# Performance work log

Hardware: AMD Instinct MI355X
Metric: run time of the kernel (lower is better)

Reference implementation:

```python
import jax, jax.numpy as jnp
import numpy as np

B, N, D, R = 4, 50000, 64, 500
E_PER = 62500
E = B * E_PER


def _build_edges():
    rng = np.random.default_rng(0)
    idx = np.repeat(np.arange(B), E_PER)
    vi = rng.integers(0, N, E)
    vj = rng.integers(0, N, E)
    order = np.lexsort((vj, vi, idx))
    idx, vi, vj = idx[order], vi[order], vj[order]
    rel = rng.integers(0, R, E)
    key_vi = idx.astype(np.int64) * N + vi
    _, idx_vi = np.unique(key_vi, return_inverse=True)  # sorted -> nondecreasing segment ids
    key_vj = idx.astype(np.int64) * N + vj
    _, idx_vj = np.unique(key_vj, return_inverse=True)
    all_keys = np.concatenate([key_vi, key_vj])
    uniq_all, inv = np.unique(all_keys, return_inverse=True)
    e2vi, e2vj = inv[:E], inv[E:]
    sel = np.stack([idx, vi, vj, rel, idx_vi, idx_vj, e2vi, e2vj], axis=1).astype(np.int32)
    return sel, int(idx_vi.max() + 1), int(idx_vj.max() + 1), int(len(uniq_all))


def setup_inputs() -> dict:
    sel, n_vi_seg, n_vj_seg, n_visited = _build_edges()
    key = jax.random.key(0)
    ks = jax.random.split(key, 9)
    na = jax.random.uniform(ks[0], (B, N), jnp.float32) + 1e-6
    na = na / jnp.sum(na, axis=1, keepdims=True)
    return {
        'node_attention': na,
        'selected_edges': jnp.asarray(sel),
        'edges_y': jax.random.uniform(ks[1], (E,), jnp.float32, 0.1, 1.0),
        'hidden_con': jax.random.normal(ks[2], (n_visited, D), jnp.float32) * 0.1,
        'hidden_uncon': jax.random.normal(ks[3], (1, N, D), jnp.float32) * 0.1,
        'rel_emb': jax.random.normal(ks[4], (R, D), jnp.float32) * 0.1,
        'ws': jax.random.normal(ks[5], (8, D), jnp.float32) * (1.0 / np.sqrt(8.0)),
        'b': jax.random.normal(ks[6], (D,), jnp.float32) * 0.01,
        'out_w': jax.random.normal(ks[7], (D,), jnp.float32) * 0.3,
        'out_b': jax.random.normal(ks[8], (D,), jnp.float32) * 0.01,
        'n_vi_seg': n_vi_seg,
        'n_vj_seg': n_vj_seg,
    }


def reference(node_attention, selected_edges, edges_y, hidden_con, hidden_uncon,
              rel_emb, ws, b, out_w, out_b, n_vi_seg, n_vj_seg):
    idx, vi, vj = selected_edges[:, 0], selected_edges[:, 1], selected_edges[:, 2]
    rel, idx_vi, idx_vj = selected_edges[:, 3], selected_edges[:, 4], selected_edges[:, 5]
    e2vi, e2vj = selected_edges[:, 6], selected_edges[:, 7]

    # Node2Edge gathers
    hc_vi, hc_vj = hidden_con[e2vi], hidden_con[e2vj]        # [E, D]
    hu = hidden_uncon[0]                                     # hidden_uncon has batch 1
    hu_vi, hu_vj = hu[vi], hu[vj]                            # [E, D]
    re = rel_emb[rel]                                        # [E, D]

    # F layer: interact = [[0,3],[0,2,3],[0,4],[0,2,4],[1,3],[1,2,3],[1,4],[1,2,4]]
    terms = (hc_vi * hc_vj, hc_vi * re * hc_vj, hc_vi * hu_vj, hc_vi * re * hu_vj,
             hu_vi * hc_vj, hu_vi * re * hc_vj, hu_vi * hu_vj, hu_vi * re * hu_vj)
    f = b
    for k in range(8):
        f = f + ws[k] * terms[k]
    f = jax.nn.relu(f) * out_w + out_b                       # [E, D]
    logits = jnp.sum(f, axis=1)                              # [E]

    # NeighborSoftmax at='vi' (segment softmax)
    seg_max = jax.ops.segment_max(logits, idx_vi, num_segments=n_vi_seg)
    e = jnp.exp(logits - seg_max[idx_vi])
    es = jax.ops.segment_sum(e, idx_vi, num_segments=n_vi_seg)
    transition = e / es[idx_vi]

    # attention flow
    na_e = node_attention[idx, vi]
    ta = na_e * transition * edges_y

    # Aggregate at='vj', sum, then scatter into (B, n_nodes)
    aggr = jax.ops.segment_sum(ta, idx_vj, num_segments=n_vj_seg)
    seg_idx = jax.ops.segment_max(idx, idx_vj, num_segments=n_vj_seg)
    seg_vj = jax.ops.segment_max(vj, idx_vj, num_segments=n_vj_seg)
    Bn, Nn = node_attention.shape
    new_att = jnp.zeros((Bn, Nn), node_attention.dtype).at[seg_idx, seg_vj].add(aggr)
    return new_att / jnp.sum(new_att, axis=1, keepdims=True)
```

## Files before the change

kernel.cpp:

```cpp
#include <hip/hip_runtime.h>
#include <math.h>

#define D 64

__global__ __launch_bounds__(256) void k_logits(
    const int* __restrict__ sel, const float* __restrict__ hc,
    const float* __restrict__ hu, const float* __restrict__ re,
    const float* __restrict__ wsm, const float* __restrict__ bias,
    const float* __restrict__ out_w, const float* __restrict__ out_b,
    float* __restrict__ logits, int* __restrict__ seg_start,
    float* __restrict__ out, float* __restrict__ row_sum,
    int E, int BN, int Bn)
{
    const int tid = blockIdx.x * 256 + threadIdx.x;
    const int nthreads = gridDim.x * 256;

    for (int i = tid; i < BN; i += nthreads) out[i] = 0.f;
    if (tid < Bn) row_sum[tid] = 0.f;

    const int lane = threadIdx.x & 63;
    const int g    = lane >> 4;
    const int d16  = lane & 15;

    const float4* wsm4 = (const float4*)wsm;
    float4 W[8];
    #pragma unroll
    for (int k = 0; k < 8; ++k) W[k] = wsm4[k * 16 + d16];
    const float4 Bv = ((const float4*)bias)[d16];
    const float4 Ow = ((const float4*)out_w)[d16];
    const float4 Ob = ((const float4*)out_b)[d16];
    const float* Wf  = (const float*)W;
    const float* Bvf = (const float*)&Bv;
    const float* Owf = (const float*)&Ow;
    const float* Obf = (const float*)&Ob;

    const float4* hc4 = (const float4*)hc;
    const float4* hu4 = (const float4*)hu;
    const float4* re4 = (const float4*)re;

    const int wave   = tid >> 6;
    const int nwaves = nthreads >> 6;
    const int octs   = (E + 7) >> 3;

    for (int q = wave; q < octs; q += nwaves) {
        const int e0 = q * 8 + g;
        const int e1 = q * 8 + 4 + g;
        const bool v0 = (e0 < E);
        const bool v1 = (e1 < E);
        const int ec0 = v0 ? e0 : (E - 1);
        const int ec1 = v1 ? e1 : (E - 1);

        const int4 sA0 = *(const int4*)(sel + (size_t)ec0 * 8);
        const int4 sB0 = *(const int4*)(sel + (size_t)ec0 * 8 + 4);
        const int4 sA1 = *(const int4*)(sel + (size_t)ec1 * 8);
        const int4 sB1 = *(const int4*)(sel + (size_t)ec1 * 8 + 4);

        const float4 a0  = hc4[(size_t)sB0.z * 16 + d16];
        const float4 c0  = hc4[(size_t)sB0.w * 16 + d16];
        const float4 ui0 = hu4[(size_t)sA0.y * 16 + d16];
        const float4 uj0 = hu4[(size_t)sA0.z * 16 + d16];
        const float4 r0  = re4[(size_t)sA0.w * 16 + d16];
        const float4 a1  = hc4[(size_t)sB1.z * 16 + d16];
        const float4 c1  = hc4[(size_t)sB1.w * 16 + d16];
        const float4 ui1 = hu4[(size_t)sA1.y * 16 + d16];
        const float4 uj1 = hu4[(size_t)sA1.z * 16 + d16];
        const float4 r1  = re4[(size_t)sA1.w * 16 + d16];

        float acc0 = 0.f, acc1 = 0.f;
        {
            const float* ap = (const float*)&a0;  const float* cp = (const float*)&c0;
            const float* up = (const float*)&ui0; const float* vp = (const float*)&uj0;
            const float* rp = (const float*)&r0;
            #pragma unroll
            for (int k4 = 0; k4 < 4; ++k4) {
                const float hcvi = ap[k4], hcvj = cp[k4], huvi = up[k4], huvj = vp[k4], rr = rp[k4];
                const float hcr = hcvi * rr, hur = huvi * rr;
                float f = Bvf[k4];
                f += Wf[0*4+k4] * (hcvi * hcvj);
                f += Wf[1*4+k4] * (hcr  * hcvj);
                f += Wf[2*4+k4] * (hcvi * huvj);
                f += Wf[3*4+k4] * (hcr  * huvj);
                f += Wf[4*4+k4] * (huvi * hcvj);
                f += Wf[5*4+k4] * (hur  * hcvj);
                f += Wf[6*4+k4] * (huvi * huvj);
                f += Wf[7*4+k4] * (hur  * huvj);
                acc0 += fmaxf(f, 0.f) * Owf[k4] + Obf[k4];
            }
        }
        {
            const float* ap = (const float*)&a1;  const float* cp = (const float*)&c1;
            const float* up = (const float*)&ui1; const float* vp = (const float*)&uj1;
            const float* rp = (const float*)&r1;
            #pragma unroll
            for (int k4 = 0; k4 < 4; ++k4) {
                const float hcvi = ap[k4], hcvj = cp[k4], huvi = up[k4], huvj = vp[k4], rr = rp[k4];
                const float hcr = hcvi * rr, hur = huvi * rr;
                float f = Bvf[k4];
                f += Wf[0*4+k4] * (hcvi * hcvj);
                f += Wf[1*4+k4] * (hcr  * hcvj);
                f += Wf[2*4+k4] * (hcvi * huvj);
                f += Wf[3*4+k4] * (hcr  * huvj);
                f += Wf[4*4+k4] * (huvi * hcvj);
                f += Wf[5*4+k4] * (hur  * hcvj);
                f += Wf[6*4+k4] * (huvi * huvj);
                f += Wf[7*4+k4] * (hur  * huvj);
                acc1 += fmaxf(f, 0.f) * Owf[k4] + Obf[k4];
            }
        }

        #pragma unroll
        for (int off = 8; off > 0; off >>= 1) {
            acc0 += __shfl_xor(acc0, off, 64);
            acc1 += __shfl_xor(acc1, off, 64);
        }

        const int idxvi0 = sB0.x, idxvi1 = sB1.x;
        const int srcm16 = (lane >= 16) ? (lane - 16) : lane;
        const int p0w = __shfl(idxvi0, srcm16, 64);
        const int p1w = __shfl(idxvi1, srcm16, 64);
        const int p1b = __shfl(idxvi0, 48 + d16, 64);

        if (d16 == 0) {
            if (v0) {
                logits[e0] = acc0;
                int prev;
                if (e0 == 0)     prev = -1;
                else if (g == 0) prev = sel[(size_t)(e0 - 1) * 8 + 4];
                else             prev = p0w;
                if (idxvi0 != prev) seg_start[idxvi0] = e0;
                if (e0 == E - 1) seg_start[idxvi0 + 1] = E;
            }
            if (v1) {
                logits[e1] = acc1;
                const int prev = (g == 0) ? p1b : p1w;
                if (idxvi1 != prev) seg_start[idxvi1] = e1;
                if (e1 == E - 1) seg_start[idxvi1 + 1] = E;
            }
        }
    }
}

__global__ __launch_bounds__(256) void k_softmax_scatter(
    const int* __restrict__ sel, const float* __restrict__ logits,
    const int* __restrict__ seg_start, const float* __restrict__ na,
    const float* __restrict__ edges_y,
    float* __restrict__ out, int E, int N)
{
    const int e = blockIdx.x * 256 + threadIdx.x;
    if (e >= E) return;

    const int4 A = *(const int4*)(sel + (size_t)e * 8);
    const int  s = sel[(size_t)e * 8 + 4];
    const int start = seg_start[s];
    const int end   = seg_start[s + 1];

    const float myl  = logits[e];
    const float na_e = na[(size_t)A.x * N + A.y];
    const float ye   = edges_y[e];

    float m = myl;
    for (int i = start; i < end; ++i) m = fmaxf(m, logits[i]);
    float sum = 0.f;
    for (int i = start; i < end; ++i) sum += __expf(logits[i] - m);

    const float ta = na_e * (__expf(myl - m) / sum) * ye;
    atomicAdd(out + (size_t)A.x * N + A.z, ta);
}

__global__ __launch_bounds__(256) void k_rowsum(
    const float4* __restrict__ out, float* __restrict__ row_sum, int N4)
{
    __shared__ float red[4];
    const int row = blockIdx.y;
    float s = 0.f;
    for (int i = blockIdx.x * 256 + threadIdx.x; i < N4; i += gridDim.x * 256) {
        const float4 v = out[(size_t)row * N4 + i];
        s += v.x + v.y + v.z + v.w;
    }
    #pragma unroll
    for (int off = 32; off > 0; off >>= 1)
        s += __shfl_xor(s, off, 64);
    if ((threadIdx.x & 63) == 0) red[threadIdx.x >> 6] = s;
    __syncthreads();
    if (threadIdx.x == 0)
        atomicAdd(row_sum + row, red[0] + red[1] + red[2] + red[3]);
}

__global__ void k_norm(float4* __restrict__ out, const float* __restrict__ row_sum, int N4) {
    const int col = blockIdx.x * blockDim.x + threadIdx.x;
    const int row = blockIdx.y;
    if (col < N4) {
        const float inv = 1.f / row_sum[row];
        const size_t i = (size_t)row * N4 + col;
        float4 v = out[i];
        v.x *= inv; v.y *= inv; v.z *= inv; v.w *= inv;
        out[i] = v;
    }
}

extern "C" void kernel_launch(void* const* d_in, const int* in_sizes, int n_in,
                              void* d_out, int out_size, void* d_ws, size_t ws_size,
                              hipStream_t stream)
{
    const float* na    = (const float*)d_in[0];
    const int*   sel   = (const int*)  d_in[1];
    const float* ey    = (const float*)d_in[2];
    const float* hc    = (const float*)d_in[3];
    const float* hu    = (const float*)d_in[4];
    const float* re    = (const float*)d_in[5];
    const float* wsm   = (const float*)d_in[6];
    const float* bias  = (const float*)d_in[7];
    const float* ow    = (const float*)d_in[8];
    const float* ob    = (const float*)d_in[9];

    float* out = (float*)d_out;

    const int E  = in_sizes[2];
    const int N  = in_sizes[4] / D;
    const int BN = in_sizes[0];
    const int Bn = BN / N;

    float* logits    = (float*)d_ws;
    int*   seg_start = (int*)  ((char*)d_ws + (size_t)E * 4);
    const size_t rs_off = (((size_t)E * 8 + 4) + 255) & ~(size_t)255;
    float* row_sum   = (float*)((char*)d_ws + rs_off);

    k_logits<<<2048, 256, 0, stream>>>(sel, hc, hu, re, wsm, bias, ow, ob,
                                       logits, seg_start, out, row_sum, E, BN, Bn);
    k_softmax_scatter<<<(E + 255) / 256, 256, 0, stream>>>(sel, logits, seg_start, na, ey,
                                                           out, E, N);
    const int N4 = N / 4;
    dim3 rgrid(16, Bn);
    k_rowsum<<<rgrid, 256, 0, stream>>>((const float4*)out, row_sum, N4);
    dim3 ngrid((N4 + 255) / 256, Bn);
    k_norm<<<ngrid, 256, 0, stream>>>((float4*)out, row_sum, N4);
}
```

Baseline: 158.9 us.

## Fuse logits and segment softmax per block with shared-memory halo window

Merges the logits kernel and the softmax-scatter kernel into one. Each block computes logits for a 256-edge chunk plus a 32-edge halo into shared memory, then does the segment softmax locally, so the global logits and seg_start arrays disappear. Row sums are accumulated through shared-memory atomics during the scatter, which removes the separate rowsum pass over the output. The cost is recomputing halo logits, a dependence on segments never crossing the chunk edge by more than 32 edges, and a separate zeroing kernel launch.

```diff
diff --git a/kernel.cpp b/kernel.cpp
--- a/kernel.cpp
+++ b/kernel.cpp
@@ -2,34 +2,49 @@
 #include <math.h>
 
 #define D 64
-
-__global__ __launch_bounds__(256) void k_logits(
+#define CH 256
+#define HALO 32
+#define WSZ (CH + HALO)
+
+__global__ void k_zero(float4* __restrict__ out4, float* __restrict__ row_sum,
+                       int BN4, int Bn)
+{
+    const int i = blockIdx.x * 256 + threadIdx.x;
+    if (i < BN4) out4[i] = make_float4(0.f, 0.f, 0.f, 0.f);
+    if (i < Bn) row_sum[i] = 0.f;
+}
+
+__global__ __launch_bounds__(256) void k_fused(
     const int* __restrict__ sel, const float* __restrict__ hc,
     const float* __restrict__ hu, const float* __restrict__ re,
     const float* __restrict__ wsm, const float* __restrict__ bias,
     const float* __restrict__ out_w, const float* __restrict__ out_b,
-    float* __restrict__ logits, int* __restrict__ seg_start,
+    const float* __restrict__ na, const float* __restrict__ edges_y,
     float* __restrict__ out, float* __restrict__ row_sum,
-    int E, int BN, int Bn)
+    int E, int N)
 {
-    const int tid = blockIdx.x * 256 + threadIdx.x;
-    const int nthreads = gridDim.x * 256;
-
-    for (int i = tid; i < BN; i += nthreads) out[i] = 0.f;
-    if (tid < Bn) row_sum[tid] = 0.f;
+    __shared__ float s_logit[WSZ];
+    __shared__ int   s_ivi[WSZ];
+    __shared__ float s_row[8];
+
+    const int b0 = blockIdx.x * CH;
+    const int Wc = min(WSZ, E - b0);
 
     const int lane = threadIdx.x & 63;
     const int g    = lane >> 4;
     const int d16  = lane & 15;
+    const int wv   = threadIdx.x >> 6;
+
+    if (threadIdx.x < 8) s_row[threadIdx.x] = 0.f;
 
     const float4* wsm4 = (const float4*)wsm;
-    float4 W[8];
+    float4 Wk[8];
     #pragma unroll
-    for (int k = 0; k < 8; ++k) W[k] = wsm4[k * 16 + d16];
+    for (int k = 0; k < 8; ++k) Wk[k] = wsm4[k * 16 + d16];
     const float4 Bv = ((const float4*)bias)[d16];
     const float4 Ow = ((const float4*)out_w)[d16];
     const float4 Ob = ((const float4*)out_b)[d16];
-    const float* Wf  = (const float*)W;
+    const float* Wf  = (const float*)Wk;
     const float* Bvf = (const float*)&Bv;
     const float* Owf = (const float*)&Ow;
     const float* Obf = (const float*)&Ob;
@@ -38,17 +53,14 @@
     const float4* hu4 = (const float4*)hu;
     const float4* re4 = (const float4*)re;
 
-    const int wave   = tid >> 6;
-    const int nwaves = nthreads >> 6;
-    const int octs   = (E + 7) >> 3;
-
-    for (int q = wave; q < octs; q += nwaves) {
-        const int e0 = q * 8 + g;
-        const int e1 = q * 8 + 4 + g;
-        const bool v0 = (e0 < E);
-        const bool v1 = (e1 < E);
-        const int ec0 = v0 ? e0 : (E - 1);
-        const int ec1 = v1 ? e1 : (E - 1);
+    #pragma unroll 1
+    for (int t = 0; t < (WSZ + 31) / 32; ++t) {
+        const int j0 = t * 32 + wv * 8 + g;
+        const int j1 = j0 + 4;
+        const bool v0 = (j0 < Wc);
+        const bool v1 = (j1 < Wc);
+        const int ec0 = v0 ? (b0 + j0) : (E - 1);
+        const int ec1 = v1 ? (b0 + j1) : (E - 1);
 
         const int4 sA0 = *(const int4*)(sel + (size_t)ec0 * 8);
         const int4 sB0 = *(const int4*)(sel + (size_t)ec0 * 8 + 4);
@@ -114,76 +126,47 @@
             acc1 += __shfl_xor(acc1, off, 64);
         }
 
-        const int idxvi0 = sB0.x, idxvi1 = sB1.x;
-        const int srcm16 = (lane >= 16) ? (lane - 16) : lane;
-        const int p0w = __shfl(idxvi0, srcm16, 64);
-        const int p1w = __shfl(idxvi1, srcm16, 64);
-        const int p1b = __shfl(idxvi0, 48 + d16, 64);
-
         if (d16 == 0) {
-            if (v0) {
-                logits[e0] = acc0;
-                int prev;
-                if (e0 == 0)     prev = -1;
-                else if (g == 0) prev = sel[(size_t)(e0 - 1) * 8 + 4];
-                else             prev = p0w;
-                if (idxvi0 != prev) seg_start[idxvi0] = e0;
-                if (e0 == E - 1) seg_start[idxvi0 + 1] = E;
-            }
-            if (v1) {
-                logits[e1] = acc1;
-                const int prev = (g == 0) ? p1b : p1w;
-                if (idxvi1 != prev) seg_start[idxvi1] = e1;
-                if (e1 == E - 1) seg_start[idxvi1 + 1] = E;
-            }
-        }
-    }
-}
-
-__global__ __launch_bounds__(256) void k_softmax_scatter(
-    const int* __restrict__ sel, const float* __restrict__ logits,
-    const int* __restrict__ seg_start, const float* __restrict__ na,
-    const float* __restrict__ edges_y,
-    float* __restrict__ out, int E, int N)
-{
-    const int e = blockIdx.x * 256 + threadIdx.x;
-    if (e >= E) return;
-
-    const int4 A = *(const int4*)(sel + (size_t)e * 8);
-    const int  s = sel[(size_t)e * 8 + 4];
-    const int start = seg_start[s];
-    const int end   = seg_start[s + 1];
-
-    const float myl  = logits[e];
-    const float na_e = na[(size_t)A.x * N + A.y];
-    const float ye   = edges_y[e];
-
-    float m = myl;
-    for (int i = start; i < end; ++i) m = fmaxf(m, logits[i]);
-    float sum = 0.f;
-    for (int i = start; i < end; ++i) sum += __expf(logits[i] - m);
-
-    const float ta = na_e * (__expf(myl - m) / sum) * ye;
-    atomicAdd(out + (size_t)A.x * N + A.z, ta);
-}
-
-__global__ __launch_bounds__(256) void k_rowsum(
-    const float4* __restrict__ out, float* __restrict__ row_sum, int N4)
-{
-    __shared__ float red[4];
-    const int row = blockIdx.y;
-    float s = 0.f;
-    for (int i = blockIdx.x * 256 + threadIdx.x; i < N4; i += gridDim.x * 256) {
-        const float4 v = out[(size_t)row * N4 + i];
-        s += v.x + v.y + v.z + v.w;
-    }
-    #pragma unroll
-    for (int off = 32; off > 0; off >>= 1)
-        s += __shfl_xor(s, off, 64);
-    if ((threadIdx.x & 63) == 0) red[threadIdx.x >> 6] = s;
+            if (v0) { s_logit[j0] = acc0; s_ivi[j0] = sB0.x; }
+            if (v1) { s_logit[j1] = acc1; s_ivi[j1] = sB1.x; }
+        }
+    }
+
     __syncthreads();
-    if (threadIdx.x == 0)
-        atomicAdd(row_sum + row, red[0] + red[1] + red[2] + red[3]);
+
+    const int ivi_prev = (b0 > 0) ? sel[((size_t)b0 - 1) * 8 + 4] : -1;
+
+    for (int j = threadIdx.x; j < Wc; j += 256) {
+        const int myivi = s_ivi[j];
+
+        int s = j;
+        while (s > 0 && s_ivi[s - 1] == myivi) --s;
+        const bool genuine = (s > 0) || (myivi != ivi_prev);
+        if (!genuine || s >= CH) continue;
+
+        int en = j + 1;
+        while (en < Wc && s_ivi[en] == myivi) ++en;
+
+        float m = s_logit[j];
+        for (int i = s; i < en; ++i) m = fmaxf(m, s_logit[i]);
+        float sum = 0.f;
+        for (int i = s; i < en; ++i) sum += __expf(s_logit[i] - m);
+
+        const int e = b0 + j;
+        const int4 A = *(const int4*)(sel + (size_t)e * 8);
+        const float ta = na[(size_t)A.x * N + A.y]
+                       * (__expf(s_logit[j] - m) / sum) * edges_y[e];
+
+        atomicAdd(out + (size_t)A.x * N + A.z, ta);
+        if (A.x < 8) atomicAdd(&s_row[A.x], ta);
+        else         atomicAdd(row_sum + A.x, ta);
+    }
+
+    __syncthreads();
+    if (threadIdx.x < 8) {
+        const float v = s_row[threadIdx.x];
+        if (v != 0.f) atomicAdd(row_sum + threadIdx.x, v);
+    }
 }
 
 __global__ void k_norm(float4* __restrict__ out, const float* __restrict__ row_sum, int N4) {
@@ -220,18 +203,17 @@
     const int BN = in_sizes[0];
     const int Bn = BN / N;
 
-    float* logits    = (float*)d_ws;
-    int*   seg_start = (int*)  ((char*)d_ws + (size_t)E * 4);
-    const size_t rs_off = (((size_t)E * 8 + 4) + 255) & ~(size_t)255;
-    float* row_sum   = (float*)((char*)d_ws + rs_off);
-
-    k_logits<<<2048, 256, 0, stream>>>(sel, hc, hu, re, wsm, bias, ow, ob,
-                                       logits, seg_start, out, row_sum, E, BN, Bn);
-    k_softmax_scatter<<<(E + 255) / 256, 256, 0, stream>>>(sel, logits, seg_start, na, ey,
-                                                           out, E, N);
-    const int N4 = N / 4;
-    dim3 rgrid(16, Bn);
-    k_rowsum<<<rgrid, 256, 0, stream>>>((const float4*)out, row_sum, N4);
+    float* row_sum = (float*)d_ws;
+
+    const int N4  = N / 4;
+    const int BN4 = BN / 4;
+
+    k_zero<<<(BN4 + 255) / 256, 256, 0, stream>>>((float4*)out, row_sum, BN4, Bn);
+
+    const int nblk = (E + CH - 1) / CH;
+    k_fused<<<nblk, 256, 0, stream>>>(sel, hc, hu, re, wsm, bias, ow, ob,
+                                      na, ey, out, row_sum, E, N);
+
     dim3 ngrid((N4 + 255) / 256, Bn);
     k_norm<<<ngrid, 256, 0, stream>>>((float4*)out, row_sum, N4);
 }
```

Result: faster. 154.7 us (-2.6%).
